# Kernel optimization log

Measured on AMD Instinct MI355X. Metric: run time of the kernel, lower is better.

Reference implementation:

```python
import jax, jax.numpy as jnp
import numpy as np

H = 4096
W = 4096
N_CELLS = H * W
ITERATIONS = 16


def setup_inputs() -> dict:
    key = jax.random.key(0)
    k1, k2 = jax.random.split(key)
    runoff = jax.random.uniform(k1, (H, W), dtype=jnp.float32)
    # each cell's downstream receiver cell (flat index into H*W grid)
    flow_idx = jax.random.randint(k2, (N_CELLS,), 0, N_CELLS, dtype=jnp.int32)
    return {
        "runoff_generated": runoff,
        "flow_direction_indices": flow_idx,
        "iterations": ITERATIONS,
    }


def reference(runoff_generated, flow_direction_indices, iterations):
    h, w = runoff_generated.shape
    current = runoff_generated.reshape(-1)   # (N,)
    accumulated = current                      # clone of initial flow

    def step(carry, _):
        accum, cur = carry
        # scatter-add: every cell pushes its current flow downstream
        accum = accum.at[flow_direction_indices].add(cur)
        cur = accum - cur
        return (accum, cur), None

    (accumulated, _), _ = jax.lax.scan(step, (accumulated, current), None, length=iterations)
    return accumulated.reshape(h, w)
```

## Files before the change

### kernel.cpp

```cpp
#include <hip/hip_runtime.h>


#define N_CELLS (1 << 24)

#define BKT_BITS 14
#define NBKT (N_CELLS >> BKT_BITS)
#define DPB (1 << BKT_BITS)
#define BKT_MASK (DPB - 1)
#define IDX_MASK (N_CELLS - 1)
#define NSUP 32
#define SUP_SHIFT 19
#define G1 256
#define BT 1024
#define EPW (N_CELLS / G1)

typedef unsigned uv4 __attribute__((ext_vector_type(4)));
typedef float fv4 __attribute__((ext_vector_type(4)));
typedef unsigned long long u64;

__device__ __align__(16) unsigned g_T[2][NBKT * G1];
__device__ __align__(16) unsigned g_bktcnt[2][NBKT];
__device__ __align__(16) unsigned g_S[2][NBKT + 4];
__device__ __align__(16) unsigned g_off1[2][NSUP * G1];
__device__ __align__(16) unsigned g_off2[2][NBKT * 8];
__device__ __align__(16) uint2 g_tmp[N_CELLS];
__device__ __align__(16) uint2 g_rec[N_CELLS];
__device__ __align__(16) int g_idx2[N_CELLS];
__device__ __align__(16) int g_idx4[N_CELLS];
__device__ __align__(16) float gB1[N_CELLS];
__device__ __align__(16) float gB2[N_CELLS];
__device__ __align__(16) float gB3[N_CELLS];
__device__ __align__(16) float gH[N_CELLS];

__device__ __forceinline__ float* sel_buf(int which, const float* r, float* dout) {
    switch (which) {
        case 0: return (float*)r;
        case 1: return gB1;
        case 2: return gB2;
        case 3: return gB3;
        case 4: return gH;
        default: return dout;
    }
}

__global__ void compose_idx(const int* __restrict__ ext, int mode) {
    const int* __restrict__ a = mode ? g_idx2 : ext;
    int* __restrict__ o = mode ? g_idx4 : g_idx2;
    int i = (blockIdx.x * 256 + threadIdx.x) * 4;
    int4 v = *reinterpret_cast<const int4*>(a + i);
    int4 r;
    r.x = a[v.x & IDX_MASK];
    r.y = a[v.y & IDX_MASK];
    r.z = a[v.z & IDX_MASK];
    r.w = a[v.w & IDX_MASK];
    *reinterpret_cast<int4*>(o + i) = r;
}

__global__ void __launch_bounds__(BT) b1_count(const int* __restrict__ ext, int set) {
    const int* __restrict__ idx = set ? g_idx4 : ext;
    __shared__ unsigned h[NBKT];
    int t = threadIdx.x;
    h[t] = 0u;
    __syncthreads();
    const uv4* p = reinterpret_cast<const uv4*>(idx) + (size_t)blockIdx.x * (EPW / 4);
    for (int k = 0; k < EPW / 4 / BT; ++k) {
        uv4 v = __builtin_nontemporal_load(&p[k * BT + t]);
        atomicAdd(&h[(v.x & IDX_MASK) >> BKT_BITS], 1u);
        atomicAdd(&h[(v.y & IDX_MASK) >> BKT_BITS], 1u);
        atomicAdd(&h[(v.z & IDX_MASK) >> BKT_BITS], 1u);
        atomicAdd(&h[(v.w & IDX_MASK) >> BKT_BITS], 1u);
    }
    __syncthreads();
    g_T[set][(size_t)t * G1 + blockIdx.x] = h[t];
}

__global__ void s1_sums(int set) {
    __shared__ unsigned sd[256];
    int t = threadIdx.x;
    sd[t] = g_T[set][(size_t)blockIdx.x * G1 + t];
    __syncthreads();
    for (int off = 128; off > 0; off >>= 1) {
        if (t < off) sd[t] += sd[t + off];
        __syncthreads();
    }
    if (t == 0) g_bktcnt[set][blockIdx.x] = sd[0];
}

__global__ void s2_scan(int set) {
    __shared__ unsigned s[256];
    int t = threadIdx.x;
    uint4 v = reinterpret_cast<const uint4*>(g_bktcnt[set])[t];
    unsigned local = v.x + v.y + v.z + v.w;
    s[t] = local;
    __syncthreads();
    for (int off = 1; off < 256; off <<= 1) {
        unsigned add = (t >= off) ? s[t - off] : 0u;
        __syncthreads();
        s[t] += add;
        __syncthreads();
    }
    unsigned run = s[t] - local;
    uint4 o;
    o.x = run; run += v.x;
    o.y = run; run += v.y;
    o.z = run; run += v.z;
    o.w = run;
    reinterpret_cast<uint4*>(g_S[set])[t] = o;
    if (t == 0) g_S[set][NBKT] = (unsigned)N_CELLS;
}

__global__ void d_off1(int set) {
    __shared__ unsigned sc[G1];
    int w = threadIdx.x;
    unsigned s = blockIdx.x;
    unsigned c = 0u;
    for (int j = 0; j < NBKT / NSUP; ++j)
        c += g_T[set][(size_t)(s * (NBKT / NSUP) + j) * G1 + w];
    sc[w] = c;
    __syncthreads();
    for (int off = 1; off < G1; off <<= 1) {
        unsigned add = (w >= off) ? sc[w - off] : 0u;
        __syncthreads();
        sc[w] += add;
        __syncthreads();
    }
    g_off1[set][(size_t)s * G1 + w] = g_S[set][s * (NBKT / NSUP)] + sc[w] - c;
}

__global__ void d_off2(int set) {
    __shared__ unsigned sd[256];
    int t = threadIdx.x;
    unsigned b = blockIdx.x;
    sd[t] = g_T[set][(size_t)b * G1 + t];
    __syncthreads();
    for (int off = 16; off > 0; off >>= 1) {
        if ((t & 31) < off) sd[t] += sd[t + off];
        __syncthreads();
    }
    if (t == 0) {
        unsigned run = g_S[set][b];
        for (int g = 0; g < 8; ++g) {
            g_off2[set][(size_t)b * 8 + g] = run;
            run += sd[g * 32];
        }
    }
}

__global__ void __launch_bounds__(BT) route1(const float* __restrict__ rin,
                                             float* __restrict__ dout,
                                             const int* __restrict__ ext,
                                             int ct_sel, int set) {
    const int* __restrict__ idx = set ? g_idx4 : ext;
    const float* __restrict__ ct = sel_buf(ct_sel, rin, dout);
    __shared__ unsigned cur[NSUP];
    int t = threadIdx.x;
    if (t < NSUP) cur[t] = g_off1[set][(size_t)t * G1 + blockIdx.x];
    __syncthreads();
    const uv4* ip = reinterpret_cast<const uv4*>(idx) + (size_t)blockIdx.x * (EPW / 4);
    const fv4* cp = reinterpret_cast<const fv4*>(ct) + (size_t)blockIdx.x * (EPW / 4);
    for (int k = 0; k < EPW / 4 / BT; ++k) {
        uv4 v = __builtin_nontemporal_load(&ip[k * BT + t]);
        fv4 c = __builtin_nontemporal_load(&cp[k * BT + t]);
        unsigned e, p;
        e = v.x & IDX_MASK; p = atomicAdd(&cur[e >> SUP_SHIFT], 1u) & IDX_MASK;
        g_tmp[p] = make_uint2(__float_as_uint(c.x), e);
        e = v.y & IDX_MASK; p = atomicAdd(&cur[e >> SUP_SHIFT], 1u) & IDX_MASK;
        g_tmp[p] = make_uint2(__float_as_uint(c.y), e);
        e = v.z & IDX_MASK; p = atomicAdd(&cur[e >> SUP_SHIFT], 1u) & IDX_MASK;
        g_tmp[p] = make_uint2(__float_as_uint(c.z), e);
        e = v.w & IDX_MASK; p = atomicAdd(&cur[e >> SUP_SHIFT], 1u) & IDX_MASK;
        g_tmp[p] = make_uint2(__float_as_uint(c.w), e);
    }
}

__global__ void __launch_bounds__(BT) route2(int set) {
    __shared__ unsigned cur[NSUP];
    unsigned wg = blockIdx.x;
    unsigned s = wg >> 3, g = wg & 7u;
    int t = threadIdx.x;
    if (t < NSUP) cur[t] = g_off2[set][(size_t)(s * NSUP + t) * 8 + g];
    __syncthreads();
    unsigned start = g_off1[set][(size_t)s * G1 + g * 32];
    unsigned end = (g < 7u) ? g_off1[set][(size_t)s * G1 + (g + 1) * 32]
                            : g_S[set][(s + 1) * NSUP];
    if (start > end) start = end;
    const u64* __restrict__ tmp = reinterpret_cast<const u64*>(g_tmp);
    unsigned e = start + t;
    for (; e + 3 * BT < end; e += 4 * BT) {
        u64 q0 = __builtin_nontemporal_load(&tmp[e]);
        u64 q1 = __builtin_nontemporal_load(&tmp[e + BT]);
        u64 q2 = __builtin_nontemporal_load(&tmp[e + 2 * BT]);
        u64 q3 = __builtin_nontemporal_load(&tmp[e + 3 * BT]);
        unsigned d0 = (unsigned)(q0 >> 32), d1 = (unsigned)(q1 >> 32);
        unsigned d2 = (unsigned)(q2 >> 32), d3 = (unsigned)(q3 >> 32);
        unsigned p0 = atomicAdd(&cur[(d0 >> BKT_BITS) & 31u], 1u) & IDX_MASK;
        unsigned p1 = atomicAdd(&cur[(d1 >> BKT_BITS) & 31u], 1u) & IDX_MASK;
        unsigned p2 = atomicAdd(&cur[(d2 >> BKT_BITS) & 31u], 1u) & IDX_MASK;
        unsigned p3 = atomicAdd(&cur[(d3 >> BKT_BITS) & 31u], 1u) & IDX_MASK;
        g_rec[p0] = make_uint2((unsigned)q0, d0);
        g_rec[p1] = make_uint2((unsigned)q1, d1);
        g_rec[p2] = make_uint2((unsigned)q2, d2);
        g_rec[p3] = make_uint2((unsigned)q3, d3);
    }
    for (; e < end; e += BT) {
        u64 q = __builtin_nontemporal_load(&tmp[e]);
        unsigned d = (unsigned)(q >> 32);
        unsigned p = atomicAdd(&cur[(d >> BKT_BITS) & 31u], 1u) & IDX_MASK;
        g_rec[p] = make_uint2((unsigned)q, d);
    }
}

__global__ void __launch_bounds__(512) acc_op(const float* __restrict__ rin,
                                              float* __restrict__ dout,
                                              int out_sel, int set, int fuse,
                                              float a0, float a1, float a2, float a3) {
    __shared__ float acc[DPB];
    int t = threadIdx.x;
    unsigned b = blockIdx.x;
    float* __restrict__ out = sel_buf(out_sel, rin, dout);
    unsigned base = g_S[set][b];
    unsigned end = g_S[set][b + 1];
    if (end > (unsigned)N_CELLS) end = (unsigned)N_CELLS;
    if (base > end) base = end;
    fv4* acc4 = reinterpret_cast<fv4*>(acc);
    fv4 z = (fv4)(0.0f);
    for (int k = 0; k < DPB / 4 / 512; ++k) acc4[k * 512 + t] = z;
    __syncthreads();
    const u64* __restrict__ rec = reinterpret_cast<const u64*>(g_rec);
    unsigned e = base + t;
    for (; e + 1536 < end; e += 2048) {
        u64 q0 = __builtin_nontemporal_load(&rec[e]);
        u64 q1 = __builtin_nontemporal_load(&rec[e + 512]);
        u64 q2 = __builtin_nontemporal_load(&rec[e + 1024]);
        u64 q3 = __builtin_nontemporal_load(&rec[e + 1536]);
        atomicAdd(&acc[(unsigned)(q0 >> 32) & BKT_MASK], __uint_as_float((unsigned)q0));
        atomicAdd(&acc[(unsigned)(q1 >> 32) & BKT_MASK], __uint_as_float((unsigned)q1));
        atomicAdd(&acc[(unsigned)(q2 >> 32) & BKT_MASK], __uint_as_float((unsigned)q2));
        atomicAdd(&acc[(unsigned)(q3 >> 32) & BKT_MASK], __uint_as_float((unsigned)q3));
    }
    for (; e < end; e += 512) {
        u64 q = __builtin_nontemporal_load(&rec[e]);
        atomicAdd(&acc[(unsigned)(q >> 32) & BKT_MASK], __uint_as_float((unsigned)q));
    }
    __syncthreads();
    size_t rowbase = (size_t)b * (DPB / 4);
    fv4* out4 = reinterpret_cast<fv4*>(out) + rowbase;
    if (fuse) {
        const fv4* r4 = reinterpret_cast<const fv4*>(rin) + rowbase;
        const fv4* p1 = reinterpret_cast<const fv4*>(gB1) + rowbase;
        const fv4* p2 = reinterpret_cast<const fv4*>(gB2) + rowbase;
        const fv4* p3 = reinterpret_cast<const fv4*>(gB3) + rowbase;
        for (int k = 0; k < DPB / 4 / 512; ++k) {
            int j = k * 512 + t;
            fv4 a = acc4[j];
            fv4 x = __builtin_nontemporal_load(&r4[j]);
            fv4 y = __builtin_nontemporal_load(&p1[j]);
            fv4 u = __builtin_nontemporal_load(&p2[j]);
            fv4 w = __builtin_nontemporal_load(&p3[j]);
            a += a0 * x + a1 * y + a2 * u + a3 * w;
            __builtin_nontemporal_store(a, &out4[j]);
        }
    } else {
        for (int k = 0; k < DPB / 4 / 512; ++k) {
            int j = k * 512 + t;
            __builtin_nontemporal_store(acc4[j], &out4[j]);
        }
    }
}

extern "C" void kernel_launch(void* const* d_in, const int* in_sizes, int n_in,
                              void* d_out, int out_size, void* d_ws, size_t ws_size,
                              hipStream_t stream) {
    const int* idx = (const int*)d_in[1];
    const float* r = (const float*)d_in[0];
    float* out = (float*)d_out;

    b1_count<<<G1, BT, 0, stream>>>(idx, 0);
    s1_sums<<<NBKT, 256, 0, stream>>>(0);
    s2_scan<<<1, 256, 0, stream>>>(0);
    d_off1<<<NSUP, G1, 0, stream>>>(0);
    d_off2<<<NBKT, 256, 0, stream>>>(0);

    compose_idx<<<N_CELLS / 4 / 256, 256, 0, stream>>>(idx, 0);
    compose_idx<<<N_CELLS / 4 / 256, 256, 0, stream>>>(idx, 1);
    b1_count<<<G1, BT, 0, stream>>>(idx, 1);
    s1_sums<<<NBKT, 256, 0, stream>>>(1);
    s2_scan<<<1, 256, 0, stream>>>(1);
    d_off1<<<NSUP, G1, 0, stream>>>(1);
    d_off2<<<NBKT, 256, 0, stream>>>(1);

    route1<<<G1, BT, 0, stream>>>(r, out, idx, 0, 0);
    route2<<<G1, BT, 0, stream>>>(0);
    acc_op<<<NBKT, 512, 0, stream>>>(r, out, 1, 0, 0, 0.f, 0.f, 0.f, 0.f);
    route1<<<G1, BT, 0, stream>>>(r, out, idx, 1, 0);
    route2<<<G1, BT, 0, stream>>>(0);
    acc_op<<<NBKT, 512, 0, stream>>>(r, out, 2, 0, 0, 0.f, 0.f, 0.f, 0.f);
    route1<<<G1, BT, 0, stream>>>(r, out, idx, 2, 0);
    route2<<<G1, BT, 0, stream>>>(0);
    acc_op<<<NBKT, 512, 0, stream>>>(r, out, 3, 0, 0, 0.f, 0.f, 0.f, 0.f);

    route1<<<G1, BT, 0, stream>>>(r, out, idx, 0, 1);
    route2<<<G1, BT, 0, stream>>>(1);
    acc_op<<<NBKT, 512, 0, stream>>>(r, out, 4, 1, 1, 91.f, 14.f, 15.f, 1.f);
    route1<<<G1, BT, 0, stream>>>(r, out, idx, 4, 1);
    route2<<<G1, BT, 0, stream>>>(1);
    acc_op<<<NBKT, 512, 0, stream>>>(r, out, 5, 1, 1, 495.f, 220.f, 286.f, 78.f);
    route1<<<G1, BT, 0, stream>>>(r, out, idx, 5, 1);
    route2<<<G1, BT, 0, stream>>>(1);
    acc_op<<<NBKT, 512, 0, stream>>>(r, out, 4, 1, 1, 210.f, 252.f, 462.f, 330.f);
    route1<<<G1, BT, 0, stream>>>(r, out, idx, 4, 1);
    route2<<<G1, BT, 0, stream>>>(1);
    acc_op<<<NBKT, 512, 0, stream>>>(r, out, 5, 1, 1, 1.f, 8.f, 36.f, 84.f);
}
```

Baseline: 2.579 ms.

## Overlap index composition and histogram with early routing iterations via tail blocks

The separate compose_idx and second b1_count launches are removed. Their work is split across extra tail workgroups appended to the route1, route2 and acc_op launches of the first three iterations, which still use the uncomposed indices. This lets the random-gather index composition run alongside the scatter and accumulate kernels instead of serially in front of them. The cost is larger grids competing for bandwidth and CUs, and carefully ordered dependencies: mode 1 composition must only start after g_idx2 is fully written.

Result: no change. 2.583 ms (+0.1%).

```diff
diff --git a/kernel.cpp b/kernel.cpp
--- a/kernel.cpp
+++ b/kernel.cpp
@@ -13,6 +13,10 @@
 #define G1 256
 #define BT 1024
 #define EPW (N_CELLS / G1)
+
+#define CSA_BLK 1638
+#define CSA_ELEMS (CSA_BLK * 4096)
+#define CSC_BLK 1640
 
 typedef unsigned uv4 __attribute__((ext_vector_type(4)));
 typedef float fv4 __attribute__((ext_vector_type(4)));
@@ -43,10 +47,12 @@
     }
 }
 
-__global__ void compose_idx(const int* __restrict__ ext, int mode) {
+
+__device__ __forceinline__ void dev_cmp(const int* __restrict__ ext, int mode,
+                                        unsigned base, unsigned tb, int t, int nthr) {
     const int* __restrict__ a = mode ? g_idx2 : ext;
     int* __restrict__ o = mode ? g_idx4 : g_idx2;
-    int i = (blockIdx.x * 256 + threadIdx.x) * 4;
+    size_t i = (size_t)base + ((size_t)tb * nthr + (unsigned)t) * 4u;
     int4 v = *reinterpret_cast<const int4*>(a + i);
     int4 r;
     r.x = a[v.x & IDX_MASK];
@@ -56,13 +62,10 @@
     *reinterpret_cast<int4*>(o + i) = r;
 }
 
-__global__ void __launch_bounds__(BT) b1_count(const int* __restrict__ ext, int set) {
-    const int* __restrict__ idx = set ? g_idx4 : ext;
-    __shared__ unsigned h[NBKT];
-    int t = threadIdx.x;
+__device__ __forceinline__ void dev_b1T(unsigned* h, unsigned wg, int t) {
     h[t] = 0u;
     __syncthreads();
-    const uv4* p = reinterpret_cast<const uv4*>(idx) + (size_t)blockIdx.x * (EPW / 4);
+    const uv4* p = reinterpret_cast<const uv4*>(g_idx4) + (size_t)wg * (EPW / 4);
     for (int k = 0; k < EPW / 4 / BT; ++k) {
         uv4 v = __builtin_nontemporal_load(&p[k * BT + t]);
         atomicAdd(&h[(v.x & IDX_MASK) >> BKT_BITS], 1u);
@@ -71,7 +74,25 @@
         atomicAdd(&h[(v.w & IDX_MASK) >> BKT_BITS], 1u);
     }
     __syncthreads();
-    g_T[set][(size_t)t * G1 + blockIdx.x] = h[t];
+    g_T[1][(size_t)t * G1 + wg] = h[t];
+}
+
+
+__global__ void __launch_bounds__(BT) b1_count(const int* __restrict__ ext) {
+    __shared__ unsigned h[NBKT];
+    int t = threadIdx.x;
+    h[t] = 0u;
+    __syncthreads();
+    const uv4* p = reinterpret_cast<const uv4*>(ext) + (size_t)blockIdx.x * (EPW / 4);
+    for (int k = 0; k < EPW / 4 / BT; ++k) {
+        uv4 v = __builtin_nontemporal_load(&p[k * BT + t]);
+        atomicAdd(&h[(v.x & IDX_MASK) >> BKT_BITS], 1u);
+        atomicAdd(&h[(v.y & IDX_MASK) >> BKT_BITS], 1u);
+        atomicAdd(&h[(v.z & IDX_MASK) >> BKT_BITS], 1u);
+        atomicAdd(&h[(v.w & IDX_MASK) >> BKT_BITS], 1u);
+    }
+    __syncthreads();
+    g_T[0][(size_t)t * G1 + blockIdx.x] = h[t];
 }
 
 __global__ void s1_sums(int set) {
@@ -146,38 +167,55 @@
     }
 }
 
+
 __global__ void __launch_bounds__(BT) route1(const float* __restrict__ rin,
                                              float* __restrict__ dout,
                                              const int* __restrict__ ext,
-                                             int ct_sel, int set) {
+                                             int ct_sel, int set,
+                                             int tailk, unsigned tail_base) {
+    __shared__ unsigned sh[NBKT];
+    unsigned b = blockIdx.x;
+    int t = threadIdx.x;
+    if (b >= (unsigned)G1) {
+        unsigned tb = b - G1;
+        if (tailk == 1) dev_cmp(ext, 0, tail_base, tb, t, BT);
+        else if (tailk == 2) dev_cmp(ext, 1, tail_base, tb, t, BT);
+        else if (tailk == 3) dev_b1T(sh, tb, t);
+        return;
+    }
     const int* __restrict__ idx = set ? g_idx4 : ext;
     const float* __restrict__ ct = sel_buf(ct_sel, rin, dout);
-    __shared__ unsigned cur[NSUP];
-    int t = threadIdx.x;
-    if (t < NSUP) cur[t] = g_off1[set][(size_t)t * G1 + blockIdx.x];
-    __syncthreads();
-    const uv4* ip = reinterpret_cast<const uv4*>(idx) + (size_t)blockIdx.x * (EPW / 4);
-    const fv4* cp = reinterpret_cast<const fv4*>(ct) + (size_t)blockIdx.x * (EPW / 4);
+    if (t < NSUP) sh[t] = g_off1[set][(size_t)t * G1 + b];
+    __syncthreads();
+    const uv4* ip = reinterpret_cast<const uv4*>(idx) + (size_t)b * (EPW / 4);
+    const fv4* cp = reinterpret_cast<const fv4*>(ct) + (size_t)b * (EPW / 4);
     for (int k = 0; k < EPW / 4 / BT; ++k) {
         uv4 v = __builtin_nontemporal_load(&ip[k * BT + t]);
         fv4 c = __builtin_nontemporal_load(&cp[k * BT + t]);
         unsigned e, p;
-        e = v.x & IDX_MASK; p = atomicAdd(&cur[e >> SUP_SHIFT], 1u) & IDX_MASK;
+        e = v.x & IDX_MASK; p = atomicAdd(&sh[e >> SUP_SHIFT], 1u) & IDX_MASK;
         g_tmp[p] = make_uint2(__float_as_uint(c.x), e);
-        e = v.y & IDX_MASK; p = atomicAdd(&cur[e >> SUP_SHIFT], 1u) & IDX_MASK;
+        e = v.y & IDX_MASK; p = atomicAdd(&sh[e >> SUP_SHIFT], 1u) & IDX_MASK;
         g_tmp[p] = make_uint2(__float_as_uint(c.y), e);
-        e = v.z & IDX_MASK; p = atomicAdd(&cur[e >> SUP_SHIFT], 1u) & IDX_MASK;
+        e = v.z & IDX_MASK; p = atomicAdd(&sh[e >> SUP_SHIFT], 1u) & IDX_MASK;
         g_tmp[p] = make_uint2(__float_as_uint(c.z), e);
-        e = v.w & IDX_MASK; p = atomicAdd(&cur[e >> SUP_SHIFT], 1u) & IDX_MASK;
+        e = v.w & IDX_MASK; p = atomicAdd(&sh[e >> SUP_SHIFT], 1u) & IDX_MASK;
         g_tmp[p] = make_uint2(__float_as_uint(c.w), e);
     }
 }
 
-__global__ void __launch_bounds__(BT) route2(int set) {
+__global__ void __launch_bounds__(BT) route2(int set, const int* __restrict__ ext,
+                                             int tailk, unsigned tail_base) {
     __shared__ unsigned cur[NSUP];
     unsigned wg = blockIdx.x;
+    int t = threadIdx.x;
+    if (wg >= (unsigned)G1) {
+        unsigned tb = wg - G1;
+        if (tailk == 1) dev_cmp(ext, 0, tail_base, tb, t, BT);
+        else if (tailk == 2) dev_cmp(ext, 1, tail_base, tb, t, BT);
+        return;
+    }
     unsigned s = wg >> 3, g = wg & 7u;
-    int t = threadIdx.x;
     if (t < NSUP) cur[t] = g_off2[set][(size_t)(s * NSUP + t) * 8 + g];
     __syncthreads();
     unsigned start = g_off1[set][(size_t)s * G1 + g * 32];
@@ -213,10 +251,18 @@
 __global__ void __launch_bounds__(512) acc_op(const float* __restrict__ rin,
                                               float* __restrict__ dout,
                                               int out_sel, int set, int fuse,
-                                              float a0, float a1, float a2, float a3) {
+                                              float a0, float a1, float a2, float a3,
+                                              const int* __restrict__ ext,
+                                              int tailk, unsigned tail_base) {
     __shared__ float acc[DPB];
     int t = threadIdx.x;
     unsigned b = blockIdx.x;
+    if (b >= (unsigned)NBKT) {
+        unsigned tb = b - NBKT;
+        if (tailk == 1) dev_cmp(ext, 0, tail_base, tb, t, 512);
+        else if (tailk == 2) dev_cmp(ext, 1, tail_base, tb, t, 512);
+        return;
+    }
     float* __restrict__ out = sel_buf(out_sel, rin, dout);
     unsigned base = g_S[set][b];
     unsigned end = g_S[set][b + 1];
@@ -274,41 +320,41 @@
     const int* idx = (const int*)d_in[1];
     const float* r = (const float*)d_in[0];
     float* out = (float*)d_out;
-
-    b1_count<<<G1, BT, 0, stream>>>(idx, 0);
+    const unsigned csB = CSA_ELEMS;
+    const unsigned csC = 2u * CSA_ELEMS;
+
+    b1_count<<<G1, BT, 0, stream>>>(idx);
     s1_sums<<<NBKT, 256, 0, stream>>>(0);
     s2_scan<<<1, 256, 0, stream>>>(0);
     d_off1<<<NSUP, G1, 0, stream>>>(0);
     d_off2<<<NBKT, 256, 0, stream>>>(0);
 
-    compose_idx<<<N_CELLS / 4 / 256, 256, 0, stream>>>(idx, 0);
-    compose_idx<<<N_CELLS / 4 / 256, 256, 0, stream>>>(idx, 1);
-    b1_count<<<G1, BT, 0, stream>>>(idx, 1);
+    route1<<<G1 + CSA_BLK, BT, 0, stream>>>(r, out, idx, 0, 0, 1, 0u);
+    route2<<<G1 + CSA_BLK, BT, 0, stream>>>(0, idx, 1, csB);
+    acc_op<<<NBKT + CSC_BLK, 512, 0, stream>>>(r, out, 1, 0, 0, 0.f, 0.f, 0.f, 0.f,
+                                               idx, 1, csC);
+    route1<<<G1 + CSA_BLK, BT, 0, stream>>>(r, out, idx, 1, 0, 2, 0u);
+    route2<<<G1 + CSA_BLK, BT, 0, stream>>>(0, idx, 2, csB);
+    acc_op<<<NBKT + CSC_BLK, 512, 0, stream>>>(r, out, 2, 0, 0, 0.f, 0.f, 0.f, 0.f,
+                                               idx, 2, csC);
+    route1<<<G1 + G1, BT, 0, stream>>>(r, out, idx, 2, 0, 3, 0u);
     s1_sums<<<NBKT, 256, 0, stream>>>(1);
     s2_scan<<<1, 256, 0, stream>>>(1);
     d_off1<<<NSUP, G1, 0, stream>>>(1);
     d_off2<<<NBKT, 256, 0, stream>>>(1);
-
-    route1<<<G1, BT, 0, stream>>>(r, out, idx, 0, 0);
-    route2<<<G1, BT, 0, stream>>>(0);
-    acc_op<<<NBKT, 512, 0, stream>>>(r, out, 1, 0, 0, 0.f, 0.f, 0.f, 0.f);
-    route1<<<G1, BT, 0, stream>>>(r, out, idx, 1, 0);
-    route2<<<G1, BT, 0, stream>>>(0);
-    acc_op<<<NBKT, 512, 0, stream>>>(r, out, 2, 0, 0, 0.f, 0.f, 0.f, 0.f);
-    route1<<<G1, BT, 0, stream>>>(r, out, idx, 2, 0);
-    route2<<<G1, BT, 0, stream>>>(0);
-    acc_op<<<NBKT, 512, 0, stream>>>(r, out, 3, 0, 0, 0.f, 0.f, 0.f, 0.f);
-
-    route1<<<G1, BT, 0, stream>>>(r, out, idx, 0, 1);
-    route2<<<G1, BT, 0, stream>>>(1);
-    acc_op<<<NBKT, 512, 0, stream>>>(r, out, 4, 1, 1, 91.f, 14.f, 15.f, 1.f);
-    route1<<<G1, BT, 0, stream>>>(r, out, idx, 4, 1);
-    route2<<<G1, BT, 0, stream>>>(1);
-    acc_op<<<NBKT, 512, 0, stream>>>(r, out, 5, 1, 1, 495.f, 220.f, 286.f, 78.f);
-    route1<<<G1, BT, 0, stream>>>(r, out, idx, 5, 1);
-    route2<<<G1, BT, 0, stream>>>(1);
-    acc_op<<<NBKT, 512, 0, stream>>>(r, out, 4, 1, 1, 210.f, 252.f, 462.f, 330.f);
-    route1<<<G1, BT, 0, stream>>>(r, out, idx, 4, 1);
-    route2<<<G1, BT, 0, stream>>>(1);
-    acc_op<<<NBKT, 512, 0, stream>>>(r, out, 5, 1, 1, 1.f, 8.f, 36.f, 84.f);
-}
+    route2<<<G1, BT, 0, stream>>>(0, idx, 0, 0u);
+    acc_op<<<NBKT, 512, 0, stream>>>(r, out, 3, 0, 0, 0.f, 0.f, 0.f, 0.f, idx, 0, 0u);
+
+    route1<<<G1, BT, 0, stream>>>(r, out, idx, 0, 1, 0, 0u);
+    route2<<<G1, BT, 0, stream>>>(1, idx, 0, 0u);
+    acc_op<<<NBKT, 512, 0, stream>>>(r, out, 4, 1, 1, 91.f, 14.f, 15.f, 1.f, idx, 0, 0u);
+    route1<<<G1, BT, 0, stream>>>(r, out, idx, 4, 1, 0, 0u);
+    route2<<<G1, BT, 0, stream>>>(1, idx, 0, 0u);
+    acc_op<<<NBKT, 512, 0, stream>>>(r, out, 5, 1, 1, 495.f, 220.f, 286.f, 78.f, idx, 0, 0u);
+    route1<<<G1, BT, 0, stream>>>(r, out, idx, 5, 1, 0, 0u);
+    route2<<<G1, BT, 0, stream>>>(1, idx, 0, 0u);
+    acc_op<<<NBKT, 512, 0, stream>>>(r, out, 4, 1, 1, 210.f, 252.f, 462.f, 330.f, idx, 0, 0u);
+    route1<<<G1, BT, 0, stream>>>(r, out, idx, 4, 1, 0, 0u);
+    route2<<<G1, BT, 0, stream>>>(1, idx, 0, 0u);
+    acc_op<<<NBKT, 512, 0, stream>>>(r, out, 5, 1, 1, 1.f, 8.f, 36.f, 84.f, idx, 0, 0u);
+}
```
